# Performance work log

Hardware: AMD Instinct MI355X
Metric: run time of the kernel (lower is better)

Reference implementation:

```python
import jax, jax.numpy as jnp
import numpy as np

SCALES = (8, 16, 32)  # matches init kwarg scale=[8,16,32]


def _pairwise_dist(x):
    # Euclidean cdist via the norm trick; clamp for numerical safety.
    sq = jnp.sum(x * x, axis=1)
    d2 = sq[:, None] + sq[None, :] - 2.0 * (x @ x.T)
    return jnp.sqrt(jnp.maximum(d2, 0.0))


def setup_inputs() -> dict:
    key = jax.random.key(0)
    k1, k2 = jax.random.split(key)
    N, D = 8192, 256
    feats_c_norm = jax.random.normal(k1, (N, D), dtype=jnp.float32)
    point_c_norm = jax.random.normal(k2, (N, 3), dtype=jnp.float32)
    f_masks = jnp.ones((N,), dtype=bool)  # all valid -> masked gather is identity (static shapes)
    return {"feats_c_norm": feats_c_norm, "point_c_norm": point_c_norm, "f_masks": f_masks}


def reference(feats_c_norm, point_c_norm, f_masks):
    # f_masks is all-True here, so feats_c_norm[f_indices] == feats_c_norm (identity).
    N = feats_c_norm.shape[0]
    dists = _pairwise_dist(point_c_norm)                     # [N, N]
    kmax = min(max(SCALES), N - 1) + 1
    # top_k of -dists gives the kmax smallest distances, sorted ascending,
    # so slicing idx[:, 1:s+1] reproduces per-scale topk(largest=False) exactly.
    _, idx = jax.lax.top_k(-dists, kmax)                     # [N, kmax] int32
    outs = [feats_c_norm]                                    # key 0 in the original dict
    for s in SCALES:
        s = min(s, N - 1)
        neighbor_feats = feats_c_norm[idx[:, 1:s + 1]]       # [N, s, D]
        outs.append(neighbor_feats.reshape(N, -1))           # [N, s*D]
    return tuple(outs)
```

## Files before the change

kernel.cpp:

```cpp
#include <hip/hip_runtime.h>

#define NPTS 8192
#define KSEL 33
#define SCAP 512

typedef float vf4 __attribute__((ext_vector_type(4)));

__global__ __launch_bounds__(256) void prep_kernel(const float* __restrict__ pts,
                                                   float4* __restrict__ pts4) {
#pragma clang fp contract(off)
    const int j = blockIdx.x * 256 + threadIdx.x;
    const float x = pts[j * 3 + 0];
    const float y = pts[j * 3 + 1];
    const float z = pts[j * 3 + 2];
    const float sq = (x * x + y * y) + z * z;
    pts4[j] = make_float4(x, y, z, sq);
}

__global__ __launch_bounds__(256) void knn_fused_kernel(const float4* __restrict__ pts4,
                                                        const float* __restrict__ feats,
                                                        float* __restrict__ out) {
#pragma clang fp contract(off)
    const int i = blockIdx.x;
    const int tid = threadIdx.x;
    const int lane = tid & 63;
    const int wv = tid >> 6;

    __shared__ unsigned red[4];
    __shared__ int sh_cnt;
    __shared__ unsigned long long S[SCAP];
    __shared__ unsigned jlist[32];

    const float4 pi = pts4[i];

    unsigned d[32];
    unsigned m1 = 0xFFFFFFFFu, m2 = 0xFFFFFFFFu;
#pragma unroll
    for (int t = 0; t < 32; ++t) {
        const int j = tid + t * 256;
        const float4 pj = pts4[j];
        const float dot = __builtin_fmaf(pi.z, pj.z, __builtin_fmaf(pi.y, pj.y, pi.x * pj.x));
        const float d2 = (pi.w + pj.w) - (2.0f * dot);
        const unsigned db = __float_as_uint(fmaxf(d2, 0.0f));
        d[t] = db;
        const unsigned mx = db > m1 ? db : m1;
        m1 = db < m1 ? db : m1;
        m2 = mx < m2 ? mx : m2;
    }
    if (tid == 0) sh_cnt = 0;

    unsigned blo = 0u, bhi = 0x7F800000u;
    while (blo < bhi) {
        const unsigned mid = (blo + bhi) >> 1;
        const int cnt = __popcll(__ballot(m1 <= mid)) + __popcll(__ballot(m2 <= mid));
        if (cnt >= KSEL) bhi = mid; else blo = mid + 1u;
    }
    if (lane == 0) red[wv] = bhi;
    __syncthreads();
    unsigned T = red[0];
    T = red[1] < T ? red[1] : T;
    T = red[2] < T ? red[2] : T;
    T = red[3] < T ? red[3] : T;

    const float s = sqrtf(__uint_as_float(T));
    const float snx = __uint_as_float(__float_as_uint(s) + 1u);
    const unsigned T2 = __float_as_uint(__fmul_rn(snx, snx)) + 2u;

    int n = 0;
#pragma unroll
    for (int t = 0; t < 32; ++t) n += (d[t] <= T2) ? 1 : 0;

    int incl = n;
#pragma unroll
    for (int sh = 1; sh < 64; sh <<= 1) {
        const int o = __shfl_up(incl, sh, 64);
        if (lane >= sh) incl += o;
    }
    int base = 0;
    if (lane == 63) base = atomicAdd(&sh_cnt, incl);
    base = __shfl(base, 63, 64);
    int ptr = base + incl - n;
#pragma unroll
    for (int t = 0; t < 32; ++t) {
        if (d[t] <= T2) {
            const unsigned db = __float_as_uint(sqrtf(__uint_as_float(d[t])));
            if (ptr < SCAP)
                S[ptr] = (((unsigned long long)db) << 32) | (unsigned)(tid + t * 256);
            ++ptr;
        }
    }
    __syncthreads();

    const int c = sh_cnt < SCAP ? sh_cnt : SCAP;
    for (int q = tid; q < c; q += 256) {
        const unsigned long long key = S[q];
        int rank = 0;
        for (int u = 0; u < c; ++u) rank += (S[u] < key) ? 1 : 0;
        if (rank >= 1 && rank < KSEL) jlist[rank - 1] = (unsigned)key;
    }
    __syncthreads();

    const unsigned long long O1 = (unsigned long long)NPTS * 256ull;
    const unsigned long long O2 = O1 + (unsigned long long)NPTS * 2048ull;
    const unsigned long long O3 = O2 + (unsigned long long)NPTS * 4096ull;

    for (int r = wv; r < 57; r += 4) {
        unsigned src;
        unsigned long long dst;
        if (r == 0) {
            src = (unsigned)i;
            dst = (unsigned long long)i * 256ull;
        } else if (r < 9) {
            const int k = r - 1;
            src = jlist[k];
            dst = O1 + (unsigned long long)i * 2048ull + (unsigned long long)k * 256ull;
        } else if (r < 25) {
            const int k = r - 9;
            src = jlist[k];
            dst = O2 + (unsigned long long)i * 4096ull + (unsigned long long)k * 256ull;
        } else {
            const int k = r - 25;
            src = jlist[k];
            dst = O3 + (unsigned long long)i * 8192ull + (unsigned long long)k * 256ull;
        }
        const vf4* s4 = (const vf4*)(feats + (unsigned long long)src * 256ull);
        vf4* d4 = (vf4*)(out + dst);
        __builtin_nontemporal_store(s4[lane], &d4[lane]);
    }
}

extern "C" void kernel_launch(void* const* d_in, const int* in_sizes, int n_in,
                              void* d_out, int out_size, void* d_ws, size_t ws_size,
                              hipStream_t stream) {
    const float* feats = (const float*)d_in[0];
    const float* pts = (const float*)d_in[1];

    float4* pts4 = (float4*)d_ws;

    prep_kernel<<<NPTS / 256, 256, 0, stream>>>(pts, pts4);
    knn_fused_kernel<<<NPTS, 256, 0, stream>>>(pts4, feats, (float*)d_out);
}
```

Baseline: 167.6 us.

## Process eight query points per block and recompute distances instead of caching

Each block now handles eight query points, so every loaded candidate point is reused across eight distance computations and the grid shrinks eightfold. Distances are no longer held in registers; they are recomputed in a second pass that compacts candidates with per-query shared atomics instead of a wave prefix scan. The gather-copy loop is software-pipelined so the next row's load is issued before the current store. The costs are more shared memory (32KB for candidates), fewer blocks to fill the GPU, serialized per-query selection, and atomic contention.

```diff
diff --git a/kernel.cpp b/kernel.cpp
--- a/kernel.cpp
+++ b/kernel.cpp
@@ -2,7 +2,9 @@
 
 #define NPTS 8192
 #define KSEL 33
-#define SCAP 512
+#define QB   8
+#define NBLK (NPTS / QB)
+#define CAPQ 512
 
 typedef float vf4 __attribute__((ext_vector_type(4)));
 
@@ -21,82 +23,92 @@
                                                         const float* __restrict__ feats,
                                                         float* __restrict__ out) {
 #pragma clang fp contract(off)
-    const int i = blockIdx.x;
+    const int i0 = blockIdx.x * QB;
     const int tid = threadIdx.x;
     const int lane = tid & 63;
     const int wv = tid >> 6;
 
-    __shared__ unsigned red[4];
-    __shared__ int sh_cnt;
-    __shared__ unsigned long long S[SCAP];
-    __shared__ unsigned jlist[32];
+    __shared__ unsigned red[4][QB];
+    __shared__ int cnt[QB];
+    __shared__ unsigned long long S[QB][CAPQ];
+    __shared__ unsigned jlist[QB][32];
 
-    const float4 pi = pts4[i];
+    float4 pi[QB];
+#pragma unroll
+    for (int q = 0; q < QB; ++q) pi[q] = pts4[i0 + q];
+    if (tid < QB) cnt[tid] = 0;
 
-    unsigned d[32];
-    unsigned m1 = 0xFFFFFFFFu, m2 = 0xFFFFFFFFu;
+    unsigned m1[QB], m2[QB];
 #pragma unroll
+    for (int q = 0; q < QB; ++q) { m1[q] = 0xFFFFFFFFu; m2[q] = 0xFFFFFFFFu; }
+
     for (int t = 0; t < 32; ++t) {
         const int j = tid + t * 256;
         const float4 pj = pts4[j];
-        const float dot = __builtin_fmaf(pi.z, pj.z, __builtin_fmaf(pi.y, pj.y, pi.x * pj.x));
-        const float d2 = (pi.w + pj.w) - (2.0f * dot);
-        const unsigned db = __float_as_uint(fmaxf(d2, 0.0f));
-        d[t] = db;
-        const unsigned mx = db > m1 ? db : m1;
-        m1 = db < m1 ? db : m1;
-        m2 = mx < m2 ? mx : m2;
+#pragma unroll
+        for (int q = 0; q < QB; ++q) {
+            const float dot = __builtin_fmaf(pi[q].z, pj.z,
+                               __builtin_fmaf(pi[q].y, pj.y, pi[q].x * pj.x));
+            const float d2 = (pi[q].w + pj.w) - (2.0f * dot);
+            const unsigned db = __float_as_uint(fmaxf(d2, 0.0f));
+            const unsigned mx = db > m1[q] ? db : m1[q];
+            m1[q] = db < m1[q] ? db : m1[q];
+            m2[q] = mx < m2[q] ? mx : m2[q];
+        }
     }
-    if (tid == 0) sh_cnt = 0;
 
-    unsigned blo = 0u, bhi = 0x7F800000u;
-    while (blo < bhi) {
-        const unsigned mid = (blo + bhi) >> 1;
-        const int cnt = __popcll(__ballot(m1 <= mid)) + __popcll(__ballot(m2 <= mid));
-        if (cnt >= KSEL) bhi = mid; else blo = mid + 1u;
+#pragma unroll
+    for (int q = 0; q < QB; ++q) {
+        unsigned blo = 0u, bhi = 0x7F800000u;
+        while (blo < bhi) {
+            const unsigned mid = (blo + bhi) >> 1;
+            const int c = __popcll(__ballot(m1[q] <= mid)) +
+                          __popcll(__ballot(m2[q] <= mid));
+            if (c >= KSEL) bhi = mid; else blo = mid + 1u;
+        }
+        if (lane == 0) red[wv][q] = bhi;
     }
-    if (lane == 0) red[wv] = bhi;
     __syncthreads();
-    unsigned T = red[0];
-    T = red[1] < T ? red[1] : T;
-    T = red[2] < T ? red[2] : T;
-    T = red[3] < T ? red[3] : T;
 
-    const float s = sqrtf(__uint_as_float(T));
-    const float snx = __uint_as_float(__float_as_uint(s) + 1u);
-    const unsigned T2 = __float_as_uint(__fmul_rn(snx, snx)) + 2u;
+    unsigned T2[QB];
+#pragma unroll
+    for (int q = 0; q < QB; ++q) {
+        unsigned T = red[0][q];
+        T = red[1][q] < T ? red[1][q] : T;
+        T = red[2][q] < T ? red[2][q] : T;
+        T = red[3][q] < T ? red[3][q] : T;
+        const float s = sqrtf(__uint_as_float(T));
+        const float snx = __uint_as_float(__float_as_uint(s) + 1u);
+        T2[q] = __float_as_uint(__fmul_rn(snx, snx)) + 2u;
+    }
 
-    int n = 0;
+    for (int t = 0; t < 32; ++t) {
+        const int j = tid + t * 256;
+        const float4 pj = pts4[j];
 #pragma unroll
-    for (int t = 0; t < 32; ++t) n += (d[t] <= T2) ? 1 : 0;
-
-    int incl = n;
-#pragma unroll
-    for (int sh = 1; sh < 64; sh <<= 1) {
-        const int o = __shfl_up(incl, sh, 64);
-        if (lane >= sh) incl += o;
-    }
-    int base = 0;
-    if (lane == 63) base = atomicAdd(&sh_cnt, incl);
-    base = __shfl(base, 63, 64);
-    int ptr = base + incl - n;
-#pragma unroll
-    for (int t = 0; t < 32; ++t) {
-        if (d[t] <= T2) {
-            const unsigned db = __float_as_uint(sqrtf(__uint_as_float(d[t])));
-            if (ptr < SCAP)
-                S[ptr] = (((unsigned long long)db) << 32) | (unsigned)(tid + t * 256);
-            ++ptr;
+        for (int q = 0; q < QB; ++q) {
+            const float dot = __builtin_fmaf(pi[q].z, pj.z,
+                               __builtin_fmaf(pi[q].y, pj.y, pi[q].x * pj.x));
+            const float d2 = (pi[q].w + pj.w) - (2.0f * dot);
+            const unsigned db = __float_as_uint(fmaxf(d2, 0.0f));
+            if (db <= T2[q]) {
+                const unsigned sb = __float_as_uint(sqrtf(__uint_as_float(db)));
+                const int pos = atomicAdd(&cnt[q], 1);
+                if (pos < CAPQ)
+                    S[q][pos] = (((unsigned long long)sb) << 32) | (unsigned)j;
+            }
         }
     }
     __syncthreads();
 
-    const int c = sh_cnt < SCAP ? sh_cnt : SCAP;
-    for (int q = tid; q < c; q += 256) {
-        const unsigned long long key = S[q];
-        int rank = 0;
-        for (int u = 0; u < c; ++u) rank += (S[u] < key) ? 1 : 0;
-        if (rank >= 1 && rank < KSEL) jlist[rank - 1] = (unsigned)key;
+    for (int q = 0; q < QB; ++q) {
+        const int cq = cnt[q] < CAPQ ? cnt[q] : CAPQ;
+        for (int u = tid; u < cq; u += 256) {
+            const unsigned long long key = S[q][u];
+            int rank = 0;
+            for (int v = 0; v < cq; ++v) rank += (S[q][v] < key) ? 1 : 0;
+            if (rank >= 1 && rank < KSEL) jlist[q][rank - 1] = (unsigned)key;
+        }
     }
     __syncthreads();
 
@@ -104,29 +116,47 @@
     const unsigned long long O2 = O1 + (unsigned long long)NPTS * 2048ull;
     const unsigned long long O3 = O2 + (unsigned long long)NPTS * 4096ull;
 
-    for (int r = wv; r < 57; r += 4) {
+    auto row_addr = [&](int r, const float4** sp, float** dp) {
+        const int q = r / 57;
+        const int rr = r - q * 57;
+        const unsigned long long i = (unsigned long long)(i0 + q);
         unsigned src;
         unsigned long long dst;
-        if (r == 0) {
+        if (rr == 0) {
             src = (unsigned)i;
-            dst = (unsigned long long)i * 256ull;
-        } else if (r < 9) {
-            const int k = r - 1;
-            src = jlist[k];
-            dst = O1 + (unsigned long long)i * 2048ull + (unsigned long long)k * 256ull;
-        } else if (r < 25) {
-            const int k = r - 9;
-            src = jlist[k];
-            dst = O2 + (unsigned long long)i * 4096ull + (unsigned long long)k * 256ull;
+            dst = i * 256ull;
+        } else if (rr < 9) {
+            const int k = rr - 1;
+            src = jlist[q][k];
+            dst = O1 + i * 2048ull + (unsigned long long)k * 256ull;
+        } else if (rr < 25) {
+            const int k = rr - 9;
+            src = jlist[q][k];
+            dst = O2 + i * 4096ull + (unsigned long long)k * 256ull;
         } else {
-            const int k = r - 25;
-            src = jlist[k];
-            dst = O3 + (unsigned long long)i * 8192ull + (unsigned long long)k * 256ull;
+            const int k = rr - 25;
+            src = jlist[q][k];
+            dst = O3 + i * 8192ull + (unsigned long long)k * 256ull;
         }
-        const vf4* s4 = (const vf4*)(feats + (unsigned long long)src * 256ull);
-        vf4* d4 = (vf4*)(out + dst);
-        __builtin_nontemporal_store(s4[lane], &d4[lane]);
+        *sp = (const float4*)(feats + (unsigned long long)src * 256ull);
+        *dp = (float*)(out + dst);
+    };
+
+    int r = wv;
+    const float4* sp;
+    float* dp;
+    row_addr(r, &sp, &dp);
+    vf4 v = ((const vf4*)sp)[lane];
+    for (; r + 4 < QB * 57; r += 4) {
+        const float4* spn;
+        float* dpn;
+        row_addr(r + 4, &spn, &dpn);
+        const vf4 vn = ((const vf4*)spn)[lane];
+        __builtin_nontemporal_store(v, &((vf4*)dp)[lane]);
+        v = vn;
+        dp = dpn;
     }
+    __builtin_nontemporal_store(v, &((vf4*)dp)[lane]);
 }
 
 extern "C" void kernel_launch(void* const* d_in, const int* in_sizes, int n_in,
@@ -138,5 +168,5 @@
     float4* pts4 = (float4*)d_ws;
 
     prep_kernel<<<NPTS / 256, 256, 0, stream>>>(pts, pts4);
-    knn_fused_kernel<<<NPTS, 256, 0, stream>>>(pts4, feats, (float*)d_out);
+    knn_fused_kernel<<<NBLK, 256, 0, stream>>>(pts4, feats, (float*)d_out);
 }
```

New measurement: 177.1 us. 5.7% more time.
